# Kernel tuning notes

Measured on AMD Instinct MI355X. Metric: run time of the kernel, lower is better.

The kernel has to match this reference:

```python
import jax, jax.numpy as jnp
import numpy as np

N, RES, C, K = 32, 256, 2, 1024
T = 1.0
EPS = 1e-6  # torch PairwiseDistance default eps added to the difference


def setup_inputs() -> dict:
    key = jax.random.key(0)
    k1, k2, k3, k4, k5, k6 = jax.random.split(key, 6)
    src_flow = jax.random.normal(k1, (N, RES, RES, C), jnp.float32)
    trg_flow = jax.random.normal(k2, (N, RES, RES, C), jnp.float32)
    # keypoints in pixel coords [0, res-1]; map_minmax + align_corners=True is identity in pixel space
    src_kp = jax.random.uniform(k3, (N, K, 2), jnp.float32) * (RES - 1)
    trg_kp = jax.random.uniform(k4, (N, K, 2), jnp.float32) * (RES - 1)
    kp_vis = jax.random.uniform(k5, (N, K)) > 0.2
    kp_wt = jax.random.uniform(k6, (N, K), jnp.float32)
    return {"src_flow": src_flow, "trg_flow": trg_flow, "src_kp": src_kp,
            "trg_kp": trg_kp, "kp_vis": kp_vis, "kp_wt": kp_wt}


def bilinear_sample(flow, kp):
    """flow: [N,H,W,C]; kp: [N,K,2] with (x,y) pixel coords. Returns [N,K,C].
    Equivalent to F.grid_sample(bilinear, padding_mode='zeros', align_corners=True)."""
    H, W = flow.shape[1], flow.shape[2]
    x, y = kp[..., 0], kp[..., 1]
    x0 = jnp.floor(x)
    y0 = jnp.floor(y)
    x1, y1 = x0 + 1.0, y0 + 1.0
    b = jnp.arange(flow.shape[0])[:, None]  # [N,1] batch index

    def gather(xi, yi):
        valid = (xi >= 0) & (xi <= W - 1) & (yi >= 0) & (yi <= H - 1)
        xc = jnp.clip(xi, 0, W - 1).astype(jnp.int32)
        yc = jnp.clip(yi, 0, H - 1).astype(jnp.int32)
        v = flow[b, yc, xc]  # [N,K,C]
        return v * valid[..., None]

    wx = (x - x0)[..., None]
    wy = (y - y0)[..., None]
    out = (gather(x0, y0) * (1 - wx) * (1 - wy)
           + gather(x1, y0) * wx * (1 - wy)
           + gather(x0, y1) * (1 - wx) * wy
           + gather(x1, y1) * wx * wy)
    return out


def _pairwise_dist(a, b):
    # a,b: [N,K,C] -> [N,K,K]; torch adds eps to the difference before norm
    d = a[:, :, None, :] - b[:, None, :, :] + EPS
    return jnp.sqrt(jnp.sum(d * d, axis=-1))


def _ce_diag(logits):
    # logits [N, K(classes), K(positions)]; label at position j is class j
    logp = jax.nn.log_softmax(logits, axis=1)
    return -jnp.diagonal(logp, axis1=1, axis2=2)  # [N,K]


def reference(src_flow, trg_flow, src_kp, trg_kp, kp_vis, kp_wt):
    src_c = bilinear_sample(src_flow, src_kp)  # [N,K,C]
    trg_c = bilinear_sample(trg_flow, trg_kp)  # [N,K,C]
    sg = jax.lax.stop_gradient
    d1 = _pairwise_dist(src_c, sg(trg_c)) * (-1.0 / T)  # [N,K,K]
    d2 = _pairwise_dist(sg(src_c), trg_c) * (-1.0 / T)
    # ignore_index=-100 on ~kp_vis zeroes those entries before weighting
    loss = (_ce_diag(d1) + _ce_diag(d2)) * kp_vis.astype(src_flow.dtype) * kp_wt
    return loss.sum() / kp_vis.sum().astype(src_flow.dtype)
```

## Files before the change

### kernel.cpp

```cpp
#include <hip/hip_runtime.h>
#include <math.h>

constexpr int   N_   = 32;
constexpr int   RES_ = 256;
constexpr int   K_   = 1024;
constexpr float EPS_ = 1e-6f;
constexpr float LOG2E_ = 1.44269504088896340736f;
constexpr float LN2_   = 0.69314718055994530942f;

constexpr int BLK_PER_N = 16;
constexpr int NBLK      = N_ * BLK_PER_N;
constexpr int NTHR      = 512;

__device__ __forceinline__ float2 gather_tex(const float* __restrict__ base, int xi, int yi) {
    bool valid = (xi >= 0) & (xi <= RES_ - 1) & (yi >= 0) & (yi <= RES_ - 1);
    int xc = min(max(xi, 0), RES_ - 1);
    int yc = min(max(yi, 0), RES_ - 1);
    float2 v = *reinterpret_cast<const float2*>(base + ((size_t)yc * RES_ + xc) * 2);
    float m = valid ? 1.0f : 0.0f;
    v.x *= m; v.y *= m;
    return v;
}

__device__ __forceinline__ float2 sample_one(const float* __restrict__ base, float2 p) {
    float x0f = floorf(p.x), y0f = floorf(p.y);
    float wx = p.x - x0f,    wy = p.y - y0f;
    int x0 = (int)x0f, y0 = (int)y0f;
    float2 v00 = gather_tex(base, x0,     y0);
    float2 v10 = gather_tex(base, x0 + 1, y0);
    float2 v01 = gather_tex(base, x0,     y0 + 1);
    float2 v11 = gather_tex(base, x0 + 1, y0 + 1);
    float w00 = (1.0f - wx) * (1.0f - wy);
    float w10 = wx * (1.0f - wy);
    float w01 = (1.0f - wx) * wy;
    float w11 = wx * wy;
    float2 o;
    o.x = v00.x * w00 + v10.x * w10 + v01.x * w01 + v11.x * w11;
    o.y = v00.y * w00 + v10.y * w10 + v01.y * w01 + v11.y * w11;
    return o;
}

__global__ void __launch_bounds__(NTHR) fused_loss_kernel(
        const float* __restrict__ src_flow, const float* __restrict__ trg_flow,
        const float* __restrict__ src_kp,   const float* __restrict__ trg_kp,
        const int*   __restrict__ kp_vis,   const float* __restrict__ kp_wt,
        float* __restrict__ partials) {
    __shared__ __align__(16) float2 s_src[K_];
    __shared__ float s_part[8][64];

    const int blk   = blockIdx.x;
    const int n     = blk >> 4;
    const int jbase = (blk & 15) * 64;
    const int t     = threadIdx.x;
    const int wave  = t >> 6;
    const int lane  = t & 63;

    const float2* skp  = reinterpret_cast<const float2*>(src_kp) + (size_t)n * K_;
    const float* sbase = src_flow + (size_t)n * RES_ * RES_ * 2;
    #pragma unroll
    for (int k = t; k < K_; k += NTHR) {
        float2 v = sample_one(sbase, skp[k]);
        v.x *= LOG2E_; v.y *= LOG2E_;
        s_src[k] = v;
    }

    const float2* tkp  = reinterpret_cast<const float2*>(trg_kp) + (size_t)n * K_;
    const float* tbase = trg_flow + (size_t)n * RES_ * RES_ * 2;
    const int j  = jbase + lane;
    float2 tc = sample_one(tbase, tkp[j]);
    const float tx = LOG2E_ * tc.x - LOG2E_ * EPS_;
    const float ty = LOG2E_ * tc.y - LOG2E_ * EPS_;

    __syncthreads();

    const float4* s4 = reinterpret_cast<const float4*>(s_src) + wave * 64;
    float s0 = 0.0f, s1 = 0.0f;
    #pragma unroll 8
    for (int k2 = 0; k2 < 64; ++k2) {
        float4 p = s4[k2];
        float dx0 = p.x - tx, dy0 = p.y - ty;
        float dx1 = p.z - tx, dy1 = p.w - ty;
        float r0 = __builtin_amdgcn_sqrtf(dx0 * dx0 + dy0 * dy0);
        float r1 = __builtin_amdgcn_sqrtf(dx1 * dx1 + dy1 * dy1);
        s0 += __builtin_amdgcn_exp2f(-r0);
        s1 += __builtin_amdgcn_exp2f(-r1);
    }
    s_part[wave][lane] = s0 + s1;
    __syncthreads();

    if (wave == 0) {
        float ssum = 0.0f;
        #pragma unroll
        for (int w = 0; w < 8; ++w) ssum += s_part[w][lane];
        float2 sj = s_src[j];
        float dxj = sj.x - tx, dyj = sj.y - ty;
        float rjj = __builtin_amdgcn_sqrtf(dxj * dxj + dyj * dyj);
        const int gj = n * K_ + j;
        float visf = kp_vis[gj] ? 1.0f : 0.0f;
        float contrib = (2.0f * LN2_) * (__builtin_amdgcn_logf(ssum) + rjj)
                        * visf * kp_wt[gj];
        float cnt = visf;
        #pragma unroll
        for (int off = 32; off > 0; off >>= 1) {
            contrib += __shfl_down(contrib, off);
            cnt     += __shfl_down(cnt, off);
        }
        if (lane == 0) {
            partials[blk * 2]     = contrib;
            partials[blk * 2 + 1] = cnt;
        }
    }
}

__global__ void __launch_bounds__(256) finalize_kernel(const float* __restrict__ partials,
                                                       float* __restrict__ out) {
    const int t = threadIdx.x;
    float v = 0.0f, c = 0.0f;
    #pragma unroll
    for (int b = t; b < NBLK; b += 256) {
        v += partials[b * 2];
        c += partials[b * 2 + 1];
    }
    #pragma unroll
    for (int off = 32; off > 0; off >>= 1) {
        v += __shfl_down(v, off);
        c += __shfl_down(c, off);
    }
    __shared__ float s_v[4], s_c[4];
    int wid = t >> 6;
    if ((t & 63) == 0) { s_v[wid] = v; s_c[wid] = c; }
    __syncthreads();
    if (t == 0) {
        out[0] = (s_v[0] + s_v[1] + s_v[2] + s_v[3]) /
                 (s_c[0] + s_c[1] + s_c[2] + s_c[3]);
    }
}

extern "C" void kernel_launch(void* const* d_in, const int* in_sizes, int n_in,
                              void* d_out, int out_size, void* d_ws, size_t ws_size,
                              hipStream_t stream) {
    const float* src_flow = (const float*)d_in[0];
    const float* trg_flow = (const float*)d_in[1];
    const float* src_kp   = (const float*)d_in[2];
    const float* trg_kp   = (const float*)d_in[3];
    const int*   kp_vis   = (const int*)d_in[4];
    const float* kp_wt    = (const float*)d_in[5];
    float* out = (float*)d_out;

    float* partials = (float*)d_ws;

    fused_loss_kernel<<<NBLK, NTHR, 0, stream>>>(src_flow, trg_flow, src_kp, trg_kp,
                                                 kp_vis, kp_wt, partials);
    finalize_kernel<<<1, 256, 0, stream>>>(partials, out);
}
```

Before: 97.73 us.

## Hoist bilinear sampling into separate kernel and fuse finalize via atomics

Adds a sample_kernel that bilinearly samples every source and target keypoint exactly once into a workspace buffer. Before, each of the 16 blocks per batch item re-sampled all 1024 source keypoints. The loss kernel now loads the presampled coordinates into shared memory. The separate finalize kernel is replaced by atomic accumulation with a last-block ticket that writes the result. The launch count stays at two, but there is an extra global round-trip for the sampled coordinates, and the float atomic accumulation order is nondeterministic.

```diff
diff --git a/kernel.cpp b/kernel.cpp
--- a/kernel.cpp
+++ b/kernel.cpp
@@ -40,12 +40,29 @@
     return o;
 }
 
-__global__ void __launch_bounds__(NTHR) fused_loss_kernel(
+__global__ void __launch_bounds__(256) sample_kernel(
         const float* __restrict__ src_flow, const float* __restrict__ trg_flow,
         const float* __restrict__ src_kp,   const float* __restrict__ trg_kp,
-        const int*   __restrict__ kp_vis,   const float* __restrict__ kp_wt,
-        float* __restrict__ partials) {
-    __shared__ __align__(16) float2 s_src[K_];
+        float2* __restrict__ src_c, float2* __restrict__ trg_c,
+        float* __restrict__ accum, int* __restrict__ flag) {
+    int gid = blockIdx.x * 256 + threadIdx.x;
+    bool is_trg = gid >= N_ * K_;
+    int idx = is_trg ? gid - N_ * K_ : gid;
+    int n = idx >> 10;
+    const float* flow = is_trg ? trg_flow : src_flow;
+    const float2* kp  = reinterpret_cast<const float2*>(is_trg ? trg_kp : src_kp);
+    float2 v = sample_one(flow + (size_t)n * RES_ * RES_ * 2, kp[idx]);
+    v.x *= LOG2E_; v.y *= LOG2E_;
+    (is_trg ? trg_c : src_c)[idx] = v;
+    if (gid == 0) { accum[0] = 0.0f; accum[1] = 0.0f; *flag = 0; }
+}
+
+__global__ void __launch_bounds__(NTHR) fused_loss_kernel(
+        const float2* __restrict__ src_c, const float2* __restrict__ trg_c,
+        const int*   __restrict__ kp_vis, const float* __restrict__ kp_wt,
+        float* __restrict__ accum, int* __restrict__ flag,
+        float* __restrict__ out) {
+    __shared__ __align__(16) float4 s_src[K_ / 2];
     __shared__ float s_part[8][64];
 
     const int blk   = blockIdx.x;
@@ -55,29 +72,21 @@
     const int wave  = t >> 6;
     const int lane  = t & 63;
 
-    const float2* skp  = reinterpret_cast<const float2*>(src_kp) + (size_t)n * K_;
-    const float* sbase = src_flow + (size_t)n * RES_ * RES_ * 2;
-    #pragma unroll
-    for (int k = t; k < K_; k += NTHR) {
-        float2 v = sample_one(sbase, skp[k]);
-        v.x *= LOG2E_; v.y *= LOG2E_;
-        s_src[k] = v;
-    }
+    const float4* g4 = reinterpret_cast<const float4*>(src_c + (size_t)n * K_);
+    s_src[t] = g4[t];
 
-    const float2* tkp  = reinterpret_cast<const float2*>(trg_kp) + (size_t)n * K_;
-    const float* tbase = trg_flow + (size_t)n * RES_ * RES_ * 2;
     const int j  = jbase + lane;
-    float2 tc = sample_one(tbase, tkp[j]);
-    const float tx = LOG2E_ * tc.x - LOG2E_ * EPS_;
-    const float ty = LOG2E_ * tc.y - LOG2E_ * EPS_;
+    const int gj = n * K_ + j;
+    float2 tc = trg_c[gj];
+    const float tx = tc.x - LOG2E_ * EPS_;
+    const float ty = tc.y - LOG2E_ * EPS_;
 
     __syncthreads();
 
-    const float4* s4 = reinterpret_cast<const float4*>(s_src) + wave * 64;
     float s0 = 0.0f, s1 = 0.0f;
     #pragma unroll 8
     for (int k2 = 0; k2 < 64; ++k2) {
-        float4 p = s4[k2];
+        float4 p = s_src[wave * 64 + k2];
         float dx0 = p.x - tx, dy0 = p.y - ty;
         float dx1 = p.z - tx, dy1 = p.w - ty;
         float r0 = __builtin_amdgcn_sqrtf(dx0 * dx0 + dy0 * dy0);
@@ -92,10 +101,9 @@
         float ssum = 0.0f;
         #pragma unroll
         for (int w = 0; w < 8; ++w) ssum += s_part[w][lane];
-        float2 sj = s_src[j];
+        float2 sj = reinterpret_cast<const float2*>(s_src)[j];
         float dxj = sj.x - tx, dyj = sj.y - ty;
         float rjj = __builtin_amdgcn_sqrtf(dxj * dxj + dyj * dyj);
-        const int gj = n * K_ + j;
         float visf = kp_vis[gj] ? 1.0f : 0.0f;
         float contrib = (2.0f * LN2_) * (__builtin_amdgcn_logf(ssum) + rjj)
                         * visf * kp_wt[gj];
@@ -106,33 +114,19 @@
             cnt     += __shfl_down(cnt, off);
         }
         if (lane == 0) {
-            partials[blk * 2]     = contrib;
-            partials[blk * 2 + 1] = cnt;
+            atomicAdd(&accum[0], contrib);
+            atomicAdd(&accum[1], cnt);
+            __threadfence();
+            int ticket = __hip_atomic_fetch_add(flag, 1, __ATOMIC_ACQ_REL,
+                                                __HIP_MEMORY_SCOPE_AGENT);
+            if (ticket == NBLK - 1) {
+                float v = __hip_atomic_load(&accum[0], __ATOMIC_RELAXED,
+                                            __HIP_MEMORY_SCOPE_AGENT);
+                float c = __hip_atomic_load(&accum[1], __ATOMIC_RELAXED,
+                                            __HIP_MEMORY_SCOPE_AGENT);
+                out[0] = v / c;
+            }
         }
-    }
-}
-
-__global__ void __launch_bounds__(256) finalize_kernel(const float* __restrict__ partials,
-                                                       float* __restrict__ out) {
-    const int t = threadIdx.x;
-    float v = 0.0f, c = 0.0f;
-    #pragma unroll
-    for (int b = t; b < NBLK; b += 256) {
-        v += partials[b * 2];
-        c += partials[b * 2 + 1];
-    }
-    #pragma unroll
-    for (int off = 32; off > 0; off >>= 1) {
-        v += __shfl_down(v, off);
-        c += __shfl_down(c, off);
-    }
-    __shared__ float s_v[4], s_c[4];
-    int wid = t >> 6;
-    if ((t & 63) == 0) { s_v[wid] = v; s_c[wid] = c; }
-    __syncthreads();
-    if (t == 0) {
-        out[0] = (s_v[0] + s_v[1] + s_v[2] + s_v[3]) /
-                 (s_c[0] + s_c[1] + s_c[2] + s_c[3]);
     }
 }
 
@@ -147,9 +141,14 @@
     const float* kp_wt    = (const float*)d_in[5];
     float* out = (float*)d_out;
 
-    float* partials = (float*)d_ws;
+    float*  ws    = (float*)d_ws;
+    float*  accum = ws;
+    int*    flag  = (int*)(ws + 2);
+    float2* src_c = (float2*)(ws + 8);
+    float2* trg_c = src_c + (size_t)N_ * K_;
 
-    fused_loss_kernel<<<NBLK, NTHR, 0, stream>>>(src_flow, trg_flow, src_kp, trg_kp,
-                                                 kp_vis, kp_wt, partials);
-    finalize_kernel<<<1, 256, 0, stream>>>(partials, out);
+    sample_kernel<<<(2 * N_ * K_) / 256, 256, 0, stream>>>(
+        src_flow, trg_flow, src_kp, trg_kp, src_c, trg_c, accum, flag);
+    fused_loss_kernel<<<NBLK, NTHR, 0, stream>>>(
+        src_c, trg_c, kp_vis, kp_wt, accum, flag, out);
 }
```

Result: slower. 111.4 us (+14.0%).
